# Kernel optimization log

Hardware: AMD Instinct MI355X
Metric: run time of the kernel (lower is better)

Reference implementation:

```python
import jax, jax.numpy as jnp
import numpy as np


def setup_inputs() -> dict:
    key = jax.random.key(0)
    ka, kb = jax.random.split(key)
    a = jax.random.normal(ka, (16384, 3), dtype=jnp.float32)
    b = jax.random.normal(kb, (16384, 3), dtype=jnp.float32)
    return {"a": a, "b": b}


def reference(a, b):
    # Pairwise squared L2 via the expansion ||a-b||^2 = ||a||^2 + ||b||^2 - 2 a.b,
    # avoiding materializing the [N, M, D] diff tensor the torch code builds.
    a2 = jnp.sum(a * a, axis=-1)                      # [N]
    b2 = jnp.sum(b * b, axis=-1)                      # [M]
    cross = jnp.einsum("nd,md->nm", a, b)             # [N, M]
    d2 = a2[:, None] + b2[None, :] - 2.0 * cross       # [N, M]
    dist = jnp.sqrt(jnp.maximum(d2, 0.0))              # clamp for numerical safety
    min_dist = jnp.min(dist, axis=1)                   # [N] nearest-neighbor dist
    return jnp.sum(min_dist)
```

## Files before the change

### kernel.cpp

```cpp
#include <hip/hip_runtime.h>
#include <math.h>


#define NPTS 16384

typedef short s16x8 __attribute__((ext_vector_type(8)));
typedef unsigned int u32x4 __attribute__((ext_vector_type(4)));
typedef float f32x16 __attribute__((ext_vector_type(16)));

__device__ __forceinline__ unsigned short f2bf(float x) {
    unsigned u = __float_as_uint(x);
    u = u + 0x7FFFu + ((u >> 16) & 1u);
    return (unsigned short)(u >> 16);
}
__device__ __forceinline__ float bf2f(unsigned short h) {
    return __uint_as_float((unsigned)h << 16);
}
__device__ __forceinline__ unsigned pk(unsigned short lo, unsigned short hi) {
    return (unsigned)lo | ((unsigned)hi << 16);
}

__global__ __launch_bounds__(256)
void cd_packb_kernel(const float* __restrict__ b,
                     u32x4* __restrict__ bcmp) {
    const int i = blockIdx.x * 256 + threadIdx.x;
    const float x = b[3 * i + 0], y = b[3 * i + 1], z = b[3 * i + 2];
    const float n2 = fmaf(x, x, fmaf(y, y, z * z));
    const unsigned short hx = f2bf(x), hy = f2bf(y), hz = f2bf(z);
    const unsigned short thx = f2bf(-2.0f * bf2f(hx));
    const unsigned short thy = f2bf(-2.0f * bf2f(hy));
    const unsigned short thz = f2bf(-2.0f * bf2f(hz));
    const unsigned short tlx = f2bf(-2.0f * (x - bf2f(hx)));
    const unsigned short tly = f2bf(-2.0f * (y - bf2f(hy)));
    const unsigned short tlz = f2bf(-2.0f * (z - bf2f(hz)));
    const unsigned short n2h = f2bf(n2), n2l = f2bf(n2 - bf2f(n2h));
    bcmp[i] = (u32x4){ pk(thx, thy), pk(thz, tlx), pk(tly, tlz), pk(n2h, n2l) };
}

__global__ __launch_bounds__(512, 4)
void cd_sweep_kernel(const float* __restrict__ a,
                     const u32x4* __restrict__ bcmp,
                     float* __restrict__ gmin) {
    __shared__ float red[8][32];
    const int tid   = threadIdx.x;
    const int lane  = tid & 63;
    const int wave  = tid >> 6;
    const int col   = lane & 31;
    const int khalf = lane >> 5;

    s16x8 af;
    {
        const int row = blockIdx.x * 32 + col;
        const float x = a[3 * row + 0];
        const float y = a[3 * row + 1];
        const float z = a[3 * row + 2];
        const float n2 = fmaf(x, x, fmaf(y, y, z * z));
        const unsigned short hx = f2bf(x), hy = f2bf(y), hz = f2bf(z);
        const unsigned short lx = f2bf(x - bf2f(hx));
        const unsigned short ly = f2bf(y - bf2f(hy));
        const unsigned short lz = f2bf(z - bf2f(hz));
        const unsigned short n2h = f2bf(n2);
        const unsigned short n2l = f2bf(n2 - bf2f(n2h));
        const unsigned short one = 0x3F80u;
        const s16x8 lo = {(short)hx, (short)hy, (short)hz, (short)hx,
                          (short)hy, (short)hz, (short)lx, (short)ly};
        const s16x8 hi = {(short)lz, (short)lx, (short)ly, (short)lz,
                          (short)n2h, (short)n2l, (short)one, (short)one};
        af = khalf ? hi : lo;
    }

    f32x16 best, zero;
    #pragma unroll
    for (int r = 0; r < 16; ++r) { best[r] = 3.4028235e38f; zero[r] = 0.0f; }

    const unsigned Kone = 0x3F803F80u;
    const u32x4* bp = bcmp + wave * 2048 + col;

    #define EXPAND(e, d)                           \
        e[0] = khalf ? d[1] : d[0];                \
        e[1] = khalf ? d[2] : d[1];                \
        e[2] = khalf ? Kone : d[2];                \
        e[3] = khalf ? d[3] : d[0];

    for (int t = 0; t < 64; t += 4) {
        const u32x4 d0 = bp[(t + 0) * 32];
        const u32x4 d1 = bp[(t + 1) * 32];
        const u32x4 d2 = bp[(t + 2) * 32];
        const u32x4 d3 = bp[(t + 3) * 32];
        u32x4 e0, e1, e2, e3;
        EXPAND(e0, d0) EXPAND(e1, d1) EXPAND(e2, d2) EXPAND(e3, d3)
        const f32x16 c0 = __builtin_amdgcn_mfma_f32_32x32x16_bf16(
            __builtin_bit_cast(s16x8, e0), af, zero, 0, 0, 0);
        const f32x16 c1 = __builtin_amdgcn_mfma_f32_32x32x16_bf16(
            __builtin_bit_cast(s16x8, e1), af, zero, 0, 0, 0);
        const f32x16 c2 = __builtin_amdgcn_mfma_f32_32x32x16_bf16(
            __builtin_bit_cast(s16x8, e2), af, zero, 0, 0, 0);
        const f32x16 c3 = __builtin_amdgcn_mfma_f32_32x32x16_bf16(
            __builtin_bit_cast(s16x8, e3), af, zero, 0, 0, 0);
        #pragma unroll
        for (int r = 0; r < 16; ++r) {
            best[r] = fminf(fminf(c0[r], c1[r]), best[r]);
            best[r] = fminf(fminf(c2[r], c3[r]), best[r]);
        }
    }
    #undef EXPAND

    float m = best[0];
    #pragma unroll
    for (int r = 1; r < 16; ++r) m = fminf(m, best[r]);
    m = fminf(m, __shfl_xor(m, 32, 64));

    if (lane < 32) red[wave][col] = m;
    __syncthreads();
    if (tid < 32) {
        float v = red[0][tid];
        #pragma unroll
        for (int w = 1; w < 8; ++w) v = fminf(v, red[w][tid]);
        gmin[blockIdx.x * 32 + tid] = fmaxf(v, 0.0f);
    }
}

__global__ __launch_bounds__(1024)
void cd_reduce_kernel(const float* __restrict__ gmin,
                      float* __restrict__ out) {
    __shared__ float red[16];
    const int tid = threadIdx.x;
    const float4* g4 = (const float4*)gmin;

    float s = 0.0f;
    #pragma unroll
    for (int i = tid; i < NPTS / 4; i += 1024) {
        const float4 v = g4[i];
        s += sqrtf(v.x) + sqrtf(v.y) + sqrtf(v.z) + sqrtf(v.w);
    }
    for (int off = 32; off > 0; off >>= 1)
        s += __shfl_down(s, off, 64);
    if ((tid & 63) == 0) red[tid >> 6] = s;
    __syncthreads();
    if (tid == 0) {
        float t = 0.0f;
        #pragma unroll
        for (int w = 0; w < 16; ++w) t += red[w];
        out[0] = t;
    }
}

extern "C" void kernel_launch(void* const* d_in, const int* in_sizes, int n_in,
                              void* d_out, int out_size, void* d_ws, size_t ws_size,
                              hipStream_t stream) {
    const float* a = (const float*)d_in[0];
    const float* b = (const float*)d_in[1];
    float* out = (float*)d_out;
    char* ws = (char*)d_ws;
    u32x4* bcmp = (u32x4*)(ws + 0);
    float* gmin = (float*)(ws + 256 * 1024);

    cd_packb_kernel<<<NPTS / 256, 256, 0, stream>>>(b, bcmp);
    cd_sweep_kernel<<<NPTS / 32, 512, 0, stream>>>(a, bcmp, gmin);
    cd_reduce_kernel<<<1, 1024, 0, stream>>>(gmin, out);
}
```

Before: 72.30 us.

## Register-block two A tiles per wave and split B sweep across block pairs

Each block now holds two 32-row A fragments and reuses every loaded B fragment for both, so each B load and expand feeds twice as many MFMAs. The B range is split in half between paired blocks, which keeps the grid size unchanged. The two partial minima per point are merged in the reduce kernel. Workspace buffers are moved to the tail of the workspace. The cost is extra accumulator registers and a larger gmin buffer.

New measurement: 69.68 us, median of 2. 1.04x faster.

```diff
diff --git a/kernel.cpp b/kernel.cpp
--- a/kernel.cpp
+++ b/kernel.cpp
@@ -37,44 +37,50 @@
     bcmp[i] = (u32x4){ pk(thx, thy), pk(thz, tlx), pk(tly, tlz), pk(n2h, n2l) };
 }
 
+__device__ __forceinline__ s16x8 make_afrag(const float* __restrict__ a,
+                                            int row, int khalf) {
+    const float x = a[3 * row + 0];
+    const float y = a[3 * row + 1];
+    const float z = a[3 * row + 2];
+    const float n2 = fmaf(x, x, fmaf(y, y, z * z));
+    const unsigned short hx = f2bf(x), hy = f2bf(y), hz = f2bf(z);
+    const unsigned short lx = f2bf(x - bf2f(hx));
+    const unsigned short ly = f2bf(y - bf2f(hy));
+    const unsigned short lz = f2bf(z - bf2f(hz));
+    const unsigned short n2h = f2bf(n2);
+    const unsigned short n2l = f2bf(n2 - bf2f(n2h));
+    const unsigned short one = 0x3F80u;
+    const s16x8 lo = {(short)hx, (short)hy, (short)hz, (short)hx,
+                      (short)hy, (short)hz, (short)lx, (short)ly};
+    const s16x8 hi = {(short)lz, (short)lx, (short)ly, (short)lz,
+                      (short)n2h, (short)n2l, (short)one, (short)one};
+    return khalf ? hi : lo;
+}
+
 __global__ __launch_bounds__(512, 4)
 void cd_sweep_kernel(const float* __restrict__ a,
                      const u32x4* __restrict__ bcmp,
                      float* __restrict__ gmin) {
-    __shared__ float red[8][32];
+    __shared__ float red[8][64];
     const int tid   = threadIdx.x;
     const int lane  = tid & 63;
     const int wave  = tid >> 6;
     const int col   = lane & 31;
     const int khalf = lane >> 5;
+    const int agroup = blockIdx.x >> 1;
+    const int g      = blockIdx.x & 1;
 
-    s16x8 af;
-    {
-        const int row = blockIdx.x * 32 + col;
-        const float x = a[3 * row + 0];
-        const float y = a[3 * row + 1];
-        const float z = a[3 * row + 2];
-        const float n2 = fmaf(x, x, fmaf(y, y, z * z));
-        const unsigned short hx = f2bf(x), hy = f2bf(y), hz = f2bf(z);
-        const unsigned short lx = f2bf(x - bf2f(hx));
-        const unsigned short ly = f2bf(y - bf2f(hy));
-        const unsigned short lz = f2bf(z - bf2f(hz));
-        const unsigned short n2h = f2bf(n2);
-        const unsigned short n2l = f2bf(n2 - bf2f(n2h));
-        const unsigned short one = 0x3F80u;
-        const s16x8 lo = {(short)hx, (short)hy, (short)hz, (short)hx,
-                          (short)hy, (short)hz, (short)lx, (short)ly};
-        const s16x8 hi = {(short)lz, (short)lx, (short)ly, (short)lz,
-                          (short)n2h, (short)n2l, (short)one, (short)one};
-        af = khalf ? hi : lo;
+    const s16x8 af0 = make_afrag(a, agroup * 64 + col, khalf);
+    const s16x8 af1 = make_afrag(a, agroup * 64 + 32 + col, khalf);
+
+    f32x16 best0, best1, zero;
+    #pragma unroll
+    for (int r = 0; r < 16; ++r) {
+        best0[r] = 3.4028235e38f; best1[r] = 3.4028235e38f; zero[r] = 0.0f;
     }
 
-    f32x16 best, zero;
-    #pragma unroll
-    for (int r = 0; r < 16; ++r) { best[r] = 3.4028235e38f; zero[r] = 0.0f; }
-
     const unsigned Kone = 0x3F803F80u;
-    const u32x4* bp = bcmp + wave * 2048 + col;
+    const u32x4* bp = bcmp + g * 8192 + wave * 1024 + col;
 
     #define EXPAND(e, d)                           \
         e[0] = khalf ? d[1] : d[0];                \
@@ -82,41 +88,52 @@
         e[2] = khalf ? Kone : d[2];                \
         e[3] = khalf ? d[3] : d[0];
 
-    for (int t = 0; t < 64; t += 4) {
+    #pragma unroll 2
+    for (int t = 0; t < 32; t += 2) {
         const u32x4 d0 = bp[(t + 0) * 32];
         const u32x4 d1 = bp[(t + 1) * 32];
-        const u32x4 d2 = bp[(t + 2) * 32];
-        const u32x4 d3 = bp[(t + 3) * 32];
-        u32x4 e0, e1, e2, e3;
-        EXPAND(e0, d0) EXPAND(e1, d1) EXPAND(e2, d2) EXPAND(e3, d3)
-        const f32x16 c0 = __builtin_amdgcn_mfma_f32_32x32x16_bf16(
-            __builtin_bit_cast(s16x8, e0), af, zero, 0, 0, 0);
-        const f32x16 c1 = __builtin_amdgcn_mfma_f32_32x32x16_bf16(
-            __builtin_bit_cast(s16x8, e1), af, zero, 0, 0, 0);
-        const f32x16 c2 = __builtin_amdgcn_mfma_f32_32x32x16_bf16(
-            __builtin_bit_cast(s16x8, e2), af, zero, 0, 0, 0);
-        const f32x16 c3 = __builtin_amdgcn_mfma_f32_32x32x16_bf16(
-            __builtin_bit_cast(s16x8, e3), af, zero, 0, 0, 0);
-        #pragma unroll
-        for (int r = 0; r < 16; ++r) {
-            best[r] = fminf(fminf(c0[r], c1[r]), best[r]);
-            best[r] = fminf(fminf(c2[r], c3[r]), best[r]);
+        u32x4 e0, e1;
+        EXPAND(e0, d0) EXPAND(e1, d1)
+        {
+            const f32x16 c0 = __builtin_amdgcn_mfma_f32_32x32x16_bf16(
+                __builtin_bit_cast(s16x8, e0), af0, zero, 0, 0, 0);
+            const f32x16 c1 = __builtin_amdgcn_mfma_f32_32x32x16_bf16(
+                __builtin_bit_cast(s16x8, e1), af0, zero, 0, 0, 0);
+            #pragma unroll
+            for (int r = 0; r < 16; ++r)
+                best0[r] = fminf(fminf(c0[r], c1[r]), best0[r]);
+        }
+        {
+            const f32x16 c0 = __builtin_amdgcn_mfma_f32_32x32x16_bf16(
+                __builtin_bit_cast(s16x8, e0), af1, zero, 0, 0, 0);
+            const f32x16 c1 = __builtin_amdgcn_mfma_f32_32x32x16_bf16(
+                __builtin_bit_cast(s16x8, e1), af1, zero, 0, 0, 0);
+            #pragma unroll
+            for (int r = 0; r < 16; ++r)
+                best1[r] = fminf(fminf(c0[r], c1[r]), best1[r]);
         }
     }
     #undef EXPAND
 
-    float m = best[0];
+    float m0 = best0[0], m1 = best1[0];
     #pragma unroll
-    for (int r = 1; r < 16; ++r) m = fminf(m, best[r]);
-    m = fminf(m, __shfl_xor(m, 32, 64));
+    for (int r = 1; r < 16; ++r) {
+        m0 = fminf(m0, best0[r]);
+        m1 = fminf(m1, best1[r]);
+    }
+    m0 = fminf(m0, __shfl_xor(m0, 32, 64));
+    m1 = fminf(m1, __shfl_xor(m1, 32, 64));
 
-    if (lane < 32) red[wave][col] = m;
+    if (lane < 32) {
+        red[wave][col]      = m0;
+        red[wave][col + 32] = m1;
+    }
     __syncthreads();
-    if (tid < 32) {
+    if (tid < 64) {
         float v = red[0][tid];
         #pragma unroll
         for (int w = 1; w < 8; ++w) v = fminf(v, red[w][tid]);
-        gmin[blockIdx.x * 32 + tid] = fmaxf(v, 0.0f);
+        gmin[g * NPTS + agroup * 64 + tid] = fmaxf(v, 0.0f);
     }
 }
 
@@ -125,13 +142,16 @@
                       float* __restrict__ out) {
     __shared__ float red[16];
     const int tid = threadIdx.x;
-    const float4* g4 = (const float4*)gmin;
+    const float4* g0 = (const float4*)gmin;
+    const float4* g1 = (const float4*)(gmin + NPTS);
 
     float s = 0.0f;
     #pragma unroll
     for (int i = tid; i < NPTS / 4; i += 1024) {
-        const float4 v = g4[i];
-        s += sqrtf(v.x) + sqrtf(v.y) + sqrtf(v.z) + sqrtf(v.w);
+        const float4 u = g0[i];
+        const float4 v = g1[i];
+        s += sqrtf(fminf(u.x, v.x)) + sqrtf(fminf(u.y, v.y)) +
+             sqrtf(fminf(u.z, v.z)) + sqrtf(fminf(u.w, v.w));
     }
     for (int off = 32; off > 0; off >>= 1)
         s += __shfl_down(s, off, 64);
@@ -152,8 +172,9 @@
     const float* b = (const float*)d_in[1];
     float* out = (float*)d_out;
     char* ws = (char*)d_ws;
-    u32x4* bcmp = (u32x4*)(ws + 0);
-    float* gmin = (float*)(ws + 256 * 1024);
+    const size_t tail = (ws_size >= (1u << 20)) ? (ws_size - (512u << 10)) : 0u;
+    u32x4* bcmp = (u32x4*)(ws + tail);
+    float* gmin = (float*)(ws + tail + 256 * 1024);
 
     cd_packb_kernel<<<NPTS / 256, 256, 0, stream>>>(b, bcmp);
     cd_sweep_kernel<<<NPTS / 32, 512, 0, stream>>>(a, bcmp, gmin);
```
